# Kernel optimization log

Hardware: AMD Instinct MI355X
Metric: run time of the kernel (lower is better)

Reference implementation:

```python
import jax, jax.numpy as jnp
import numpy as np

N = 50000   # nodes
E = 800000  # edges (avg degree 16)
H = 256     # hidden_dim
OUT = 256   # out_dim


def _leaky(x, slope=0.01):
    return jnp.where(x >= 0, x, slope * x)


def _mlp3(x, W1, b1, W2, b2, W3, b3):
    # MLP(hidden, hidden/2, hidden/2, hidden) with LeakyReLU(0.01) between layers
    x = _leaky(x @ W1 + b1)
    x = _leaky(x @ W2 + b2)
    return x @ W3 + b3


def setup_inputs() -> dict:
    key = jax.random.key(0)
    ks = jax.random.split(key, 16)
    Hh = H // 2

    def w(k, i, o):
        return (jax.random.normal(k, (i, o), jnp.float32) / np.float32(np.sqrt(i)))

    return {
        'h': jax.random.normal(ks[0], (N, H), jnp.float32),
        'src': jax.random.randint(ks[1], (E,), 0, N, dtype=jnp.int32),
        'dst': jax.random.randint(ks[2], (E,), 0, N, dtype=jnp.int32),
        'r': jax.random.randint(ks[3], (E,), 0, 2, dtype=jnp.int32),
        'inv': jax.random.randint(ks[4], (N,), 0, 2, dtype=jnp.int32),
        'inv_W1': w(ks[5], H, Hh), 'inv_b1': jnp.zeros((Hh,), jnp.float32),
        'inv_W2': w(ks[6], Hh, Hh), 'inv_b2': jnp.zeros((Hh,), jnp.float32),
        'inv_W3': w(ks[7], Hh, H), 'inv_b3': jnp.zeros((H,), jnp.float32),
        'and_W1': w(ks[8], H, Hh), 'and_b1': jnp.zeros((Hh,), jnp.float32),
        'and_W2': w(ks[9], Hh, Hh), 'and_b2': jnp.zeros((Hh,), jnp.float32),
        'and_W3': w(ks[10], Hh, H), 'and_b3': jnp.zeros((H,), jnp.float32),
        'proj_W1': w(ks[11], H, H), 'proj_b1': jnp.zeros((H,), jnp.float32),
        'proj_W2': w(ks[12], H, OUT), 'proj_b2': jnp.zeros((OUT,), jnp.float32),
    }


def reference(h, src, dst, r, inv,
              inv_W1, inv_b1, inv_W2, inv_b2, inv_W3, inv_b3,
              and_W1, and_b1, and_W2, and_b2, and_W3, and_b3,
              proj_W1, proj_b1, proj_W2, proj_b2):
    # edge_msg: gather src features, apply func_inv on edges with r == 1
    msg = h[src]  # [E, H]
    msg = jnp.where((r == 1)[:, None],
                    _mlp3(msg, inv_W1, inv_b1, inv_W2, inv_b2, inv_W3, inv_b3),
                    msg)
    # fn.mean('m', 'neigh'): mean over incoming edges per destination node
    sums = jax.ops.segment_sum(msg, dst, num_segments=N)          # [N, H]
    cnt = jax.ops.segment_sum(jnp.ones((E,), msg.dtype), dst, num_segments=N)
    neigh = sums / jnp.maximum(cnt, 1.0)[:, None]
    # apply_nodes_func: func_and, then func_inv where inv flag set
    res = _mlp3(neigh, and_W1, and_b1, and_W2, and_b2, and_W3, and_b3)
    res = jnp.where((inv == 1)[:, None],
                    _mlp3(res, inv_W1, inv_b1, inv_W2, inv_b2, inv_W3, inv_b3),
                    res)
    # proj_head: MLP(H, H, OUT) with negative_slope=0 (i.e. ReLU)
    out = jax.nn.relu(res @ proj_W1 + proj_b1) @ proj_W2 + proj_b2
    return out
```

## Files before the change

### kernel.cpp

```cpp
#include <hip/hip_runtime.h>

typedef _Float16 f16_t;
typedef f16_t f16x2 __attribute__((ext_vector_type(2)));
typedef f16_t f16x4 __attribute__((ext_vector_type(4)));
typedef f16_t f16x8 __attribute__((ext_vector_type(8)));
typedef float f32x4 __attribute__((ext_vector_type(4)));
typedef float f32x16 __attribute__((ext_vector_type(16)));

#define MFMA16H(a, b, c) __builtin_amdgcn_mfma_f32_16x16x32_f16(a, b, c, 0, 0, 0)
#define MFMA32H(a, b, c) __builtin_amdgcn_mfma_f32_32x32x16_f16(a, b, c, 0, 0, 0)

__device__ __forceinline__ float leaky01(float v) { return v >= 0.f ? v : 0.01f * v; }

__device__ __forceinline__ void acc_f16x4(float& s0, float& s1, float& s2, float& s3,
                                          f16x4 v)
{
#if __has_builtin(__builtin_amdgcn_fdot2)
    const f16x2 K10 = (f16x2){(f16_t)1.0f, (f16_t)0.0f};
    const f16x2 K01 = (f16x2){(f16_t)0.0f, (f16_t)1.0f};
    f16x2 lo = (f16x2){v.x, v.y};
    f16x2 hi = (f16x2){v.z, v.w};
    s0 = __builtin_amdgcn_fdot2(lo, K10, s0, false);
    s1 = __builtin_amdgcn_fdot2(lo, K01, s1, false);
    s2 = __builtin_amdgcn_fdot2(hi, K10, s2, false);
    s3 = __builtin_amdgcn_fdot2(hi, K01, s3, false);
#else
    s0 += (float)v.x; s1 += (float)v.y; s2 += (float)v.z; s3 += (float)v.w;
#endif
}

#define OFF_IW1 0
#define OFF_IW2 32768
#define OFF_IW3 49152
#define OFF_AW1 81920
#define OFF_AW2 114688
#define OFF_AW3 131072
#define OFF_PW1 163840
#define OFF_PW2 229376
#define OFF_M3  294912
#define WP_TOTAL 311296

template<int KD, int NC>
__device__ __forceinline__ void gemm16(
    const f16_t* __restrict__ a, int sa, const f16_t* __restrict__ B,
    int cb, int qd, int ln, f32x4 (&acc)[4])
{
#pragma unroll
    for (int rt = 0; rt < 4; ++rt) acc[rt] = (f32x4){0.f, 0.f, 0.f, 0.f};
#pragma unroll
    for (int k0 = 0; k0 < KD; k0 += 32) {
        int ka = k0 + qd * 8;
        f16x8 b = *(const f16x8*)(B + ((size_t)((k0 >> 5) * 4 + qd) * NC + cb + ln) * 8);
        f16x8 a0 = *(const f16x8*)&a[ln * sa + ka];
        f16x8 a1 = *(const f16x8*)&a[(16 + ln) * sa + ka];
        f16x8 a2 = *(const f16x8*)&a[(32 + ln) * sa + ka];
        f16x8 a3 = *(const f16x8*)&a[(48 + ln) * sa + ka];
        acc[0] = MFMA16H(a0, b, acc[0]);
        acc[1] = MFMA16H(a1, b, acc[1]);
        acc[2] = MFMA16H(a2, b, acc[2]);
        acc[3] = MFMA16H(a3, b, acc[3]);
    }
}

template<int KD, int NC>
__device__ __forceinline__ void gemm32(
    const f16_t* __restrict__ a, int sa, const f16_t* __restrict__ B,
    int cb, int l31, int kh, f32x16 &o0, f32x16 &o1)
{
    f32x16 c0, c1;
#pragma unroll
    for (int i = 0; i < 16; ++i) { c0[i] = 0.f; c1[i] = 0.f; }
    const int ar0 = l31 * sa + kh * 8;
    const int ar1 = (32 + l31) * sa + kh * 8;
    const int bcol = cb + l31;
#pragma unroll
    for (int kc = 0; kc < KD; kc += 32) {
        f16x8 b0 = *(const f16x8*)(B + ((size_t)((kc >> 3) + kh) * NC + bcol) * 8);
        f16x8 b1 = *(const f16x8*)(B + ((size_t)((kc >> 3) + 2 + kh) * NC + bcol) * 8);
        f16x8 a00 = *(const f16x8*)&a[ar0 + kc];
        f16x8 a01 = *(const f16x8*)&a[ar0 + kc + 16];
        f16x8 a10 = *(const f16x8*)&a[ar1 + kc];
        f16x8 a11 = *(const f16x8*)&a[ar1 + kc + 16];
        c0 = MFMA32H(a00, b0, c0);
        c1 = MFMA32H(a10, b0, c1);
        c0 = MFMA32H(a01, b1, c0);
        c1 = MFMA32H(a11, b1, c1);
    }
    o0 = c0; o1 = c1;
}

template<int ACT>
__device__ __forceinline__ void epi16(
    f32x4 (&acc)[4], const float* __restrict__ bias,
    int cb, int qd, int ln, f16_t* d, int stride)
{
    int col = cb + ln;
    float bb = bias[col];
#pragma unroll
    for (int rt = 0; rt < 4; ++rt)
#pragma unroll
        for (int r = 0; r < 4; ++r) {
            float v = acc[rt][r] + bb;
            if (ACT == 1) v = leaky01(v);
            else if (ACT == 2) v = fmaxf(v, 0.f);
            d[(rt * 16 + qd * 4 + r) * stride + col] = (f16_t)v;
        }
}

template<int ACT>
__device__ __forceinline__ void epi32(
    const f32x16 &a0, const f32x16 &a1, const float* __restrict__ bias,
    int cb, int l31, int kh, f16_t* d, int stride)
{
    int col = cb + l31;
    float bb = bias[col];
#pragma unroll
    for (int r = 0; r < 16; ++r) {
        float v0 = a0[r] + bb;
        float v1 = a1[r] + bb;
        if (ACT == 1) { v0 = leaky01(v0); v1 = leaky01(v1); }
        else if (ACT == 2) { v0 = fmaxf(v0, 0.f); v1 = fmaxf(v1, 0.f); }
        int row = (r & 3) + 8 * (r >> 2) + 4 * kh;
        d[row * stride + col] = (f16_t)v0;
        d[(32 + row) * stride + col] = (f16_t)v1;
    }
}

__global__ __launch_bounds__(512, 4) void kernelA(
    const float* __restrict__ h, f16_t* __restrict__ zbuf,
    const f16_t* __restrict__ wp, const float* __restrict__ ib1,
    const float* __restrict__ ib2, const float* __restrict__ c3f, int M,
    int tiles, const int* __restrict__ dstE, int* __restrict__ cnt, int E)
{
    __shared__ f16_t X[64][264];
    __shared__ f16_t Y[64][136];

    const int tid = threadIdx.x;

    if ((int)blockIdx.x >= tiles) {
        int e = (blockIdx.x - tiles) * 512 + tid;
        if (e < E) atomicAdd(&cnt[dstE[e]], 1);
        return;
    }

    const int row0 = blockIdx.x * 64;
    const int lane = tid & 63;
    const int wv = tid >> 6;
    const int qd = lane >> 4;
    const int ln = lane & 15;
    const int cb = wv * 16;
    const int l31 = lane & 31;
    const int kh = lane >> 5;

    {
        const float4* src4 = (const float4*)(h + (size_t)row0 * 256);
#pragma unroll
        for (int i = 0; i < 8; ++i) {
            int q = i * 512 + tid;
            int row = q >> 6;
            int kc = (q & 63) * 4;
            float4 v = make_float4(0.f, 0.f, 0.f, 0.f);
            if (row0 + row < M) v = src4[q];
            *(f16x4*)&X[row][kc] = (f16x4){(f16_t)v.x, (f16_t)v.y, (f16_t)v.z, (f16_t)v.w};
        }
    }
    __syncthreads();

    {
        const bool isz = wv < 4;
        const int cb32 = (wv & 3) * 32;
        const f16_t* Bw = wp + (isz ? OFF_AW1 : OFF_IW1);
        f32x16 z0, z1;
        gemm32<256, 128>(&X[0][0], 264, Bw, cb32, l31, kh, z0, z1);
        int col = cb32 + l31;
        if (isz) {
#pragma unroll
            for (int r = 0; r < 16; ++r) {
                int lrow = (r & 3) + 8 * (r >> 2) + 4 * kh;
                int row = row0 + lrow;
                if (row < M) zbuf[((size_t)row * 2) * 128 + col] = (f16_t)z0[r];
                row += 32;
                if (row < M) zbuf[((size_t)row * 2) * 128 + col] = (f16_t)z1[r];
            }
        } else {
            float bb = ib1[col];
#pragma unroll
            for (int r = 0; r < 16; ++r) {
                int lrow = (r & 3) + 8 * (r >> 2) + 4 * kh;
                Y[lrow][col] = (f16_t)leaky01(z0[r] + bb);
                Y[32 + lrow][col] = (f16_t)leaky01(z1[r] + bb);
            }
        }
    }
    __syncthreads();

    f32x4 a4[4];

    gemm16<128, 128>(&Y[0][0], 136, wp + OFF_IW2, cb, qd, ln, a4);
    epi16<1>(a4, ib2, cb, qd, ln, &X[0][0], 264);
    __syncthreads();

    gemm16<128, 128>(&X[0][0], 264, wp + OFF_M3, cb, qd, ln, a4);
    {
        int col = cb + ln;
        float bb = c3f[col];
#pragma unroll
        for (int rt = 0; rt < 4; ++rt)
#pragma unroll
            for (int r = 0; r < 4; ++r) {
                int row = row0 + rt * 16 + qd * 4 + r;
                if (row < M) zbuf[((size_t)row * 2 + 1) * 128 + col] = (f16_t)(a4[rt][r] + bb);
            }
    }
}

__global__ __launch_bounds__(512, 4) void kernelB(
    const f16_t* __restrict__ zbuf, const int* __restrict__ ridx,
    const int* __restrict__ offs, const int* __restrict__ cnt,
    const float* __restrict__ ab1, const int* __restrict__ invf,
    float* __restrict__ out, const f16_t* __restrict__ wp,
    const float* __restrict__ ab2, const float* __restrict__ ab3,
    const float* __restrict__ ib1, const float* __restrict__ ib2,
    const float* __restrict__ ib3, const float* __restrict__ pb1,
    const float* __restrict__ pb2, int M)
{
    __shared__ f16_t C[64][264];
    __shared__ f16_t A[64][136];
    __shared__ int sflag[64];

    const int tid = threadIdx.x;
    const int row0 = blockIdx.x * 64;
    const int lane = tid & 63;
    const int wv = tid >> 6;
    const int qd = lane >> 4;
    const int ln = lane & 15;
    const int cb2 = wv * 16;
    const int l31 = lane & 31;
    const int kh = lane >> 5;
    const int cb32 = wv * 32;

    const int hw = tid >> 5;
    const int hl = tid & 31;
    const int hbase = lane & 32;
    const f16x4* zp4 = (const f16x4*)zbuf;

#pragma unroll
    for (int pass = 0; pass < 4; ++pass) {
        int nl = pass * 16 + hw;
        int row = row0 + nl;
        float s0 = 0.f, s1 = 0.f, s2 = 0.f, s3 = 0.f;
        int c = 0;
        if (row < M) {
            int beg = offs[row];
            c = cnt[row];
            for (int base = 0; base < c; base += 32) {
                int rem = c - base; if (rem > 32) rem = 32;
                int myr = (hl < rem) ? ridx[beg + base + hl] : 0;
                int j = 0;
                for (; j + 16 <= rem; j += 16) {
                    f16x4 v[16];
#pragma unroll
                    for (int i = 0; i < 16; ++i) {
                        int rr = __shfl(myr, hbase + j + i);
                        v[i] = zp4[(size_t)rr * 32 + hl];
                    }
#pragma unroll
                    for (int i = 0; i < 16; ++i)
                        acc_f16x4(s0, s1, s2, s3, v[i]);
                }
                for (; j + 8 <= rem; j += 8) {
                    f16x4 v[8];
#pragma unroll
                    for (int i = 0; i < 8; ++i) {
                        int rr = __shfl(myr, hbase + j + i);
                        v[i] = zp4[(size_t)rr * 32 + hl];
                    }
#pragma unroll
                    for (int i = 0; i < 8; ++i)
                        acc_f16x4(s0, s1, s2, s3, v[i]);
                }
                for (; j < rem; ++j) {
                    int rr = __shfl(myr, hbase + j);
                    f16x4 vv = zp4[(size_t)rr * 32 + hl];
                    acc_f16x4(s0, s1, s2, s3, vv);
                }
            }
        }
        float invc = 1.0f / fmaxf((float)c, 1.0f);
        float4 bv = *(const float4*)&ab1[hl * 4];
        float m0 = leaky01(s0 * invc + bv.x);
        float m1 = leaky01(s1 * invc + bv.y);
        float m2 = leaky01(s2 * invc + bv.z);
        float m3 = leaky01(s3 * invc + bv.w);
        *(f16x4*)&A[nl][hl * 4] = (f16x4){(f16_t)m0, (f16_t)m1, (f16_t)m2, (f16_t)m3};
    }
    if (tid < 64) {
        int rr = row0 + tid;
        sflag[tid] = (rr < M) ? invf[rr] : 0;
    }
    __syncthreads();

    f32x4 a4[4];
    f32x16 c0, c1;

    gemm16<128, 128>(&A[0][0], 136, wp + OFF_AW2, cb2, qd, ln, a4);
    __syncthreads();
    epi16<1>(a4, ab2, cb2, qd, ln, &A[0][0], 136);
    __syncthreads();

    gemm32<128, 256>(&A[0][0], 136, wp + OFF_AW3, cb32, l31, kh, c0, c1);
    epi32<0>(c0, c1, ab3, cb32, l31, kh, &C[0][0], 264);
    __syncthreads();

    gemm16<256, 128>(&C[0][0], 264, wp + OFF_IW1, cb2, qd, ln, a4);
    epi16<1>(a4, ib1, cb2, qd, ln, &A[0][0], 136);
    __syncthreads();

    gemm16<128, 128>(&A[0][0], 136, wp + OFF_IW2, cb2, qd, ln, a4);
    __syncthreads();
    epi16<1>(a4, ib2, cb2, qd, ln, &A[0][0], 136);
    __syncthreads();

    gemm32<128, 256>(&A[0][0], 136, wp + OFF_IW3, cb32, l31, kh, c0, c1);
    {
        int col = cb32 + l31;
        float bb = ib3[col];
#pragma unroll
        for (int r = 0; r < 16; ++r) {
            int lrow = (r & 3) + 8 * (r >> 2) + 4 * kh;
            if (sflag[lrow] == 1) C[lrow][col] = (f16_t)(c0[r] + bb);
            if (sflag[32 + lrow] == 1) C[32 + lrow][col] = (f16_t)(c1[r] + bb);
        }
    }
    __syncthreads();

    gemm32<256, 256>(&C[0][0], 264, wp + OFF_PW1, cb32, l31, kh, c0, c1);
    __syncthreads();
    epi32<2>(c0, c1, pb1, cb32, l31, kh, &C[0][0], 264);
    __syncthreads();

    gemm32<256, 256>(&C[0][0], 264, wp + OFF_PW2, cb32, l31, kh, c0, c1);
    {
        int col = cb32 + l31;
        float bb = pb2[col];
#pragma unroll
        for (int r = 0; r < 16; ++r) {
            int lrow = (r & 3) + 8 * (r >> 2) + 4 * kh;
            int row = row0 + lrow;
            if (row < M) out[(size_t)row * 256 + col] = c0[r] + bb;
            row += 32;
            if (row < M) out[(size_t)row * 256 + col] = c1[r] + bb;
        }
    }
}

__global__ void mc3_kernel(const float* __restrict__ iW3, const float* __restrict__ aW1,
                           const float* __restrict__ ib3, float* __restrict__ m3f,
                           float* __restrict__ c3f)
{
    int b = blockIdx.x;
    if (b < 64) {
        int idx = b * 256 + threadIdx.x;
        int k = idx >> 7, j = idx & 127;
        float s = 0.f;
        for (int t = 0; t < 256; ++t) s += iW3[k * 256 + t] * aW1[t * 128 + j];
        m3f[idx] = s;
    } else {
        int j = threadIdx.x;
        if (j < 128) {
            float s = 0.f;
            for (int t = 0; t < 256; ++t) s += ib3[t] * aW1[t * 128 + j];
            c3f[j] = s;
        }
    }
}

__global__ void pack_all(const float* s0, const float* s1, const float* s2,
                         const float* s3, const float* s4, const float* s5,
                         const float* s6, const float* s7, const float* s8,
                         f16_t* dst)
{
    const float* srcs[9] = {s0, s1, s2, s3, s4, s5, s6, s7, s8};
    const int lgN[9] = {7, 7, 8, 7, 7, 8, 8, 8, 7};
    const int sz[9]  = {32768, 16384, 32768, 32768, 16384, 32768, 65536, 65536, 16384};
    const int off[9] = {OFF_IW1, OFF_IW2, OFF_IW3, OFF_AW1, OFF_AW2, OFF_AW3,
                        OFF_PW1, OFF_PW2, OFF_M3};
    int m = blockIdx.y;
    int idx = blockIdx.x * blockDim.x + threadIdx.x;
    if (idx >= sz[m]) return;
    int lg = lgN[m];
    int Nc = 1 << lg;
    int k = idx >> lg;
    int n = idx & (Nc - 1);
    int p = ((k >> 3) * Nc + n) * 8 + (k & 7);
    dst[off[m] + p] = (f16_t)srcs[m][idx];
}

__global__ void scan1(const int* __restrict__ cnt, int* __restrict__ offs,
                      int* __restrict__ bsum, int Nn)
{
    __shared__ int s[256];
    int tid = threadIdx.x;
    int g = blockIdx.x * 256 + tid;
    int v = (g < Nn) ? cnt[g] : 0;
    s[tid] = v;
    __syncthreads();
    for (int off = 1; off < 256; off <<= 1) {
        int u = (tid >= off) ? s[tid - off] : 0;
        __syncthreads();
        s[tid] += u;
        __syncthreads();
    }
    if (g < Nn) offs[g] = s[tid] - v;
    if (tid == 255) bsum[blockIdx.x] = s[255];
}

__global__ void scan2(int* __restrict__ bsum, int NB)
{
    __shared__ int s[256];
    int tid = threadIdx.x;
    if (NB > 256) {
        if (tid == 0) {
            int run = 0;
            for (int i = 0; i < NB; ++i) { int v = bsum[i]; bsum[i] = run; run += v; }
        }
        return;
    }
    int v = (tid < NB) ? bsum[tid] : 0;
    s[tid] = v;
    __syncthreads();
    for (int off = 1; off < 256; off <<= 1) {
        int u = (tid >= off) ? s[tid - off] : 0;
        __syncthreads();
        s[tid] += u;
        __syncthreads();
    }
    if (tid < NB) bsum[tid] = s[tid] - v;
}

__global__ void scan3(int* __restrict__ offs, const int* __restrict__ bsum,
                      int* __restrict__ cursor, int Nn)
{
    int g = blockIdx.x * 256 + threadIdx.x;
    if (g < Nn) {
        int o = offs[g] + bsum[blockIdx.x];
        offs[g] = o;
        cursor[g] = o;
    }
}

__global__ void fill_kernel(const int* __restrict__ dst, const int* __restrict__ src,
                            const int* __restrict__ r, int* __restrict__ cursor,
                            int* __restrict__ ridx, int E)
{
    int e = blockIdx.x * blockDim.x + threadIdx.x;
    if (e < E) {
        int p = atomicAdd(&cursor[dst[e]], 1);
        ridx[p] = src[e] * 2 + r[e];
    }
}

extern "C" void kernel_launch(void* const* d_in, const int* in_sizes, int n_in,
                              void* d_out, int out_size, void* d_ws, size_t ws_size,
                              hipStream_t stream)
{
    const float* h   = (const float*)d_in[0];
    const int* src   = (const int*)d_in[1];
    const int* dst   = (const int*)d_in[2];
    const int* r     = (const int*)d_in[3];
    const int* inv   = (const int*)d_in[4];
    const float* iW1 = (const float*)d_in[5];
    const float* ib1 = (const float*)d_in[6];
    const float* iW2 = (const float*)d_in[7];
    const float* ib2 = (const float*)d_in[8];
    const float* iW3 = (const float*)d_in[9];
    const float* ib3 = (const float*)d_in[10];
    const float* aW1 = (const float*)d_in[11];
    const float* ab1 = (const float*)d_in[12];
    const float* aW2 = (const float*)d_in[13];
    const float* ab2 = (const float*)d_in[14];
    const float* aW3 = (const float*)d_in[15];
    const float* ab3 = (const float*)d_in[16];
    const float* pW1 = (const float*)d_in[17];
    const float* pb1 = (const float*)d_in[18];
    const float* pW2 = (const float*)d_in[19];
    const float* pb2 = (const float*)d_in[20];

    const int N = in_sizes[0] / 256;
    const int E = in_sizes[1];
    float* out = (float*)d_out;

    f16_t* zbuf = (f16_t*)d_ws;
    int* cnt    = (int*)(zbuf + (size_t)2 * N * 128);
    int* offs   = cnt + N;
    int* cursor = offs + N;
    int* bsum   = cursor + N;
    int* ridx   = bsum + 256;
    f16_t* wp   = (f16_t*)(ridx + E);
    float* m3f  = (float*)(wp + WP_TOTAL);
    float* c3f  = m3f + 16384;

    (void)hipMemsetAsync(cnt, 0, (size_t)N * sizeof(int), stream);

    mc3_kernel<<<65, 256, 0, stream>>>(iW3, aW1, ib3, m3f, c3f);
    pack_all<<<dim3(256, 9), 256, 0, stream>>>(iW1, iW2, iW3, aW1, aW2, aW3,
                                               pW1, pW2, m3f, wp);

    const int tiles = (N + 63) / 64;
    const int EB = (E + 511) / 512;
    const int NB = (N + 255) / 256;

    kernelA<<<tiles + EB, 512, 0, stream>>>(h, zbuf, wp, ib1, ib2, c3f, N,
                                            tiles, dst, cnt, E);

    scan1<<<NB, 256, 0, stream>>>(cnt, offs, bsum, N);
    scan2<<<1, 256, 0, stream>>>(bsum, NB);
    scan3<<<NB, 256, 0, stream>>>(offs, bsum, cursor, N);
    fill_kernel<<<(E + 255) / 256, 256, 0, stream>>>(dst, src, r, cursor, ridx, E);

    kernelB<<<tiles, 512, 0, stream>>>(zbuf, ridx, offs, cnt, ab1, inv, out, wp,
                                       ab2, ab3, ib1, ib2, ib3, pb1, pb2, N);
}
```

Baseline: 339.3 us.

## Stage zbuf writes through LDS and merge small setup kernels

KernelA now stages both halves of each node's zbuf row in shared memory and writes them out as coalesced 16-byte vectors, replacing scattered 2-byte stores. The mc3 product computation is folded into the weight-packing kernel, writing the packed f16 result directly. scan2 and scan3 are merged into a single kernel that redoes the block-sum scan in every block when NB<=256. Together these cut launch count and improve store efficiency, at the cost of an extra barrier and reuse of X/Y shared buffers.

```diff
diff --git a/kernel.cpp b/kernel.cpp
--- a/kernel.cpp
+++ b/kernel.cpp
@@ -172,15 +172,14 @@
         const f16_t* Bw = wp + (isz ? OFF_AW1 : OFF_IW1);
         f32x16 z0, z1;
         gemm32<256, 128>(&X[0][0], 264, Bw, cb32, l31, kh, z0, z1);
+        __syncthreads();
         int col = cb32 + l31;
         if (isz) {
 #pragma unroll
             for (int r = 0; r < 16; ++r) {
                 int lrow = (r & 3) + 8 * (r >> 2) + 4 * kh;
-                int row = row0 + lrow;
-                if (row < M) zbuf[((size_t)row * 2) * 128 + col] = (f16_t)z0[r];
-                row += 32;
-                if (row < M) zbuf[((size_t)row * 2) * 128 + col] = (f16_t)z1[r];
+                X[lrow][128 + col] = (f16_t)z0[r];
+                X[32 + lrow][128 + col] = (f16_t)z1[r];
             }
         } else {
             float bb = ib1[col];
@@ -207,10 +206,22 @@
 #pragma unroll
         for (int rt = 0; rt < 4; ++rt)
 #pragma unroll
-            for (int r = 0; r < 4; ++r) {
-                int row = row0 + rt * 16 + qd * 4 + r;
-                if (row < M) zbuf[((size_t)row * 2 + 1) * 128 + col] = (f16_t)(a4[rt][r] + bb);
-            }
+            for (int r = 0; r < 4; ++r)
+                Y[rt * 16 + qd * 4 + r][col] = (f16_t)(a4[rt][r] + bb);
+    }
+    __syncthreads();
+
+#pragma unroll
+    for (int i = 0; i < 4; ++i) {
+        int q = i * 512 + tid;
+        int node = q >> 5;
+        int seg = q & 31;
+        int row = row0 + node;
+        if (row < M) {
+            f16x8 v = (seg < 16) ? *(const f16x8*)&X[node][128 + seg * 8]
+                                 : *(const f16x8*)&Y[node][(seg - 16) * 8];
+            *(f16x8*)&zbuf[(size_t)row * 256 + seg * 8] = v;
+        }
     }
 }
 
@@ -354,39 +365,38 @@
     }
 }
 
-__global__ void mc3_kernel(const float* __restrict__ iW3, const float* __restrict__ aW1,
-                           const float* __restrict__ ib3, float* __restrict__ m3f,
-                           float* __restrict__ c3f)
-{
-    int b = blockIdx.x;
-    if (b < 64) {
-        int idx = b * 256 + threadIdx.x;
-        int k = idx >> 7, j = idx & 127;
-        float s = 0.f;
-        for (int t = 0; t < 256; ++t) s += iW3[k * 256 + t] * aW1[t * 128 + j];
-        m3f[idx] = s;
-    } else {
-        int j = threadIdx.x;
-        if (j < 128) {
+__global__ void pack_mc3(const float* s0, const float* s1, const float* s2,
+                         const float* s3, const float* s4, const float* s5,
+                         const float* s6, const float* s7,
+                         const float* __restrict__ ib3, f16_t* dst,
+                         float* __restrict__ c3f)
+{
+    int m = blockIdx.y;
+    int bx = blockIdx.x;
+    if (m == 8) {
+        if (bx < 64) {
+            int idx = bx * 256 + threadIdx.x;
+            int k = idx >> 7, j = idx & 127;
             float s = 0.f;
-            for (int t = 0; t < 256; ++t) s += ib3[t] * aW1[t * 128 + j];
-            c3f[j] = s;
-        }
-    }
-}
-
-__global__ void pack_all(const float* s0, const float* s1, const float* s2,
-                         const float* s3, const float* s4, const float* s5,
-                         const float* s6, const float* s7, const float* s8,
-                         f16_t* dst)
-{
-    const float* srcs[9] = {s0, s1, s2, s3, s4, s5, s6, s7, s8};
-    const int lgN[9] = {7, 7, 8, 7, 7, 8, 8, 8, 7};
-    const int sz[9]  = {32768, 16384, 32768, 32768, 16384, 32768, 65536, 65536, 16384};
-    const int off[9] = {OFF_IW1, OFF_IW2, OFF_IW3, OFF_AW1, OFF_AW2, OFF_AW3,
-                        OFF_PW1, OFF_PW2, OFF_M3};
-    int m = blockIdx.y;
-    int idx = blockIdx.x * blockDim.x + threadIdx.x;
+            for (int t = 0; t < 256; ++t) s += s2[k * 256 + t] * s3[t * 128 + j];
+            int p = ((k >> 3) * 128 + j) * 8 + (k & 7);
+            dst[OFF_M3 + p] = (f16_t)s;
+        } else if (bx == 64) {
+            int j = threadIdx.x;
+            if (j < 128) {
+                float s = 0.f;
+                for (int t = 0; t < 256; ++t) s += ib3[t] * s3[t * 128 + j];
+                c3f[j] = s;
+            }
+        }
+        return;
+    }
+    const float* srcs[8] = {s0, s1, s2, s3, s4, s5, s6, s7};
+    const int lgN[8] = {7, 7, 8, 7, 7, 8, 8, 8};
+    const int sz[8]  = {32768, 16384, 32768, 32768, 16384, 32768, 65536, 65536};
+    const int off[8] = {OFF_IW1, OFF_IW2, OFF_IW3, OFF_AW1, OFF_AW2, OFF_AW3,
+                        OFF_PW1, OFF_PW2};
+    int idx = bx * blockDim.x + threadIdx.x;
     if (idx >= sz[m]) return;
     int lg = lgN[m];
     int Nc = 1 << lg;
@@ -415,17 +425,12 @@
     if (tid == 255) bsum[blockIdx.x] = s[255];
 }
 
-__global__ void scan2(int* __restrict__ bsum, int NB)
+__global__ void scan3b(int* __restrict__ offs, const int* __restrict__ bsum,
+                       int* __restrict__ cursor, int Nn, int NB)
 {
     __shared__ int s[256];
     int tid = threadIdx.x;
-    if (NB > 256) {
-        if (tid == 0) {
-            int run = 0;
-            for (int i = 0; i < NB; ++i) { int v = bsum[i]; bsum[i] = run; run += v; }
-        }
-        return;
-    }
+    int bid = blockIdx.x;
     int v = (tid < NB) ? bsum[tid] : 0;
     s[tid] = v;
     __syncthreads();
@@ -435,7 +440,21 @@
         s[tid] += u;
         __syncthreads();
     }
-    if (tid < NB) bsum[tid] = s[tid] - v;
+    int base = (bid > 0) ? s[bid - 1] : 0;
+    int g = bid * 256 + tid;
+    if (g < Nn) {
+        int o = offs[g] + base;
+        offs[g] = o;
+        cursor[g] = o;
+    }
+}
+
+__global__ void scan2(int* __restrict__ bsum, int NB)
+{
+    if (threadIdx.x == 0) {
+        int run = 0;
+        for (int i = 0; i < NB; ++i) { int v = bsum[i]; bsum[i] = run; run += v; }
+    }
 }
 
 __global__ void scan3(int* __restrict__ offs, const int* __restrict__ bsum,
@@ -497,14 +516,12 @@
     int* bsum   = cursor + N;
     int* ridx   = bsum + 256;
     f16_t* wp   = (f16_t*)(ridx + E);
-    float* m3f  = (float*)(wp + WP_TOTAL);
-    float* c3f  = m3f + 16384;
+    float* c3f  = (float*)(wp + WP_TOTAL);
 
     (void)hipMemsetAsync(cnt, 0, (size_t)N * sizeof(int), stream);
 
-    mc3_kernel<<<65, 256, 0, stream>>>(iW3, aW1, ib3, m3f, c3f);
-    pack_all<<<dim3(256, 9), 256, 0, stream>>>(iW1, iW2, iW3, aW1, aW2, aW3,
-                                               pW1, pW2, m3f, wp);
+    pack_mc3<<<dim3(256, 9), 256, 0, stream>>>(iW1, iW2, iW3, aW1, aW2, aW3,
+                                               pW1, pW2, ib3, wp, c3f);
 
     const int tiles = (N + 63) / 64;
     const int EB = (E + 511) / 512;
@@ -514,8 +531,12 @@
                                             tiles, dst, cnt, E);
 
     scan1<<<NB, 256, 0, stream>>>(cnt, offs, bsum, N);
-    scan2<<<1, 256, 0, stream>>>(bsum, NB);
-    scan3<<<NB, 256, 0, stream>>>(offs, bsum, cursor, N);
+    if (NB <= 256) {
+        scan3b<<<NB, 256, 0, stream>>>(offs, bsum, cursor, N, NB);
+    } else {
+        scan2<<<1, 1, 0, stream>>>(bsum, NB);
+        scan3<<<NB, 256, 0, stream>>>(offs, bsum, cursor, N);
+    }
     fill_kernel<<<(E + 255) / 256, 256, 0, stream>>>(dst, src, r, cursor, ridx, E);
 
     kernelB<<<tiles, 512, 0, stream>>>(zbuf, ridx, offs, cnt, ab1, inv, out, wp,
```

Measured after the change: 339.2 us. No clear change (-0.0%).
